# Performance work log

Measured on AMD Instinct MI355X. Metric: run time of the kernel, lower is better.

Reference implementation:

```python
import jax, jax.numpy as jnp
import numpy as np

B, T, D_MODEL = 2, 2048, 2048
N_HEADS, N_KV = 16, 8
HEAD_DIM = D_MODEL // N_HEADS  # 128
EPS = 1e-6


def rmsnorm(x, g):
    # qwen-compatible: compute in fp32, scale by learned weight
    xf = x.astype(jnp.float32)
    var = jnp.mean(xf * xf, axis=-1, keepdims=True)
    return (xf * jax.lax.rsqrt(var + EPS) * g).astype(x.dtype)


def apply_rope(x, cos, sin):
    # x: [b, h, t, d]; cos/sin: [t, d]
    d = x.shape[-1]
    x1, x2 = x[..., : d // 2], x[..., d // 2 :]
    rotated = jnp.concatenate([-x2, x1], axis=-1)
    return x * cos[None, None, :, :] + rotated * sin[None, None, :, :]


def setup_inputs() -> dict:
    key = jax.random.key(0)
    ks = jax.random.split(key, 8)
    x = jax.random.normal(ks[0], (B, T, D_MODEL), dtype=jnp.float32)
    # causal mask: True = masked out
    mask = jnp.triu(jnp.ones((T, T), dtype=bool), k=1)
    # rope tables
    inv_freq = 1.0 / (1e6 ** (np.arange(0, HEAD_DIM, 2, dtype=np.float32) / HEAD_DIM))
    angles = np.arange(T, dtype=np.float32)[:, None] * inv_freq[None, :]  # [T, d/2]
    angles = np.concatenate([angles, angles], axis=1)  # [T, d]
    cos = jnp.asarray(np.cos(angles), dtype=jnp.float32)
    sin = jnp.asarray(np.sin(angles), dtype=jnp.float32)
    s = 0.02
    Wq = jax.random.normal(ks[1], (D_MODEL, D_MODEL), dtype=jnp.float32) * s
    Wk = jax.random.normal(ks[2], (N_KV * HEAD_DIM, D_MODEL), dtype=jnp.float32) * s
    Wv = jax.random.normal(ks[3], (N_KV * HEAD_DIM, D_MODEL), dtype=jnp.float32) * s
    Wo = jax.random.normal(ks[4], (D_MODEL, D_MODEL), dtype=jnp.float32) * s
    bo = jnp.zeros((D_MODEL,), dtype=jnp.float32)
    gq = jnp.ones((HEAD_DIM,), dtype=jnp.float32)
    gk = jnp.ones((HEAD_DIM,), dtype=jnp.float32)
    return {"x": x, "mask": mask, "cos": cos, "sin": sin, "Wq": Wq, "Wk": Wk,
            "Wv": Wv, "Wo": Wo, "bo": bo, "gq": gq, "gk": gk}


def reference(x, mask, cos, sin, Wq, Wk, Wv, Wo, bo, gq, gk):
    b, t, _ = x.shape
    # projections
    q = (x @ Wq.T).reshape(b, t, N_HEADS, HEAD_DIM)
    q = rmsnorm(q, gq).transpose(0, 2, 1, 3)          # [b, H, t, d]
    q = apply_rope(q, cos[:t], sin[:t])
    k = (x @ Wk.T).reshape(b, t, N_KV, HEAD_DIM)
    k = rmsnorm(k, gk).transpose(0, 2, 1, 3)          # [b, G, t, d]
    k = apply_rope(k, cos[:t], sin[:t])
    v = (x @ Wv.T).reshape(b, t, N_KV, HEAD_DIM).transpose(0, 2, 1, 3)
    # GQA broadcast of KV heads
    rep = N_HEADS // N_KV
    k = jnp.repeat(k, rep, axis=1)                    # [b, H, t, d]
    v = jnp.repeat(v, rep, axis=1)
    scores = jnp.einsum("bhqd,bhkd->bhqk", q, k)
    scores = jnp.where(mask[:t, :t][None, None], -jnp.inf, scores)
    attn = jax.nn.softmax(scores / jnp.sqrt(jnp.float32(HEAD_DIM)), axis=-1)
    out = jnp.einsum("bhqk,bhkd->bqhd", attn, v).reshape(b, t, N_HEADS * HEAD_DIM)
    return out @ Wo.T + bo
```

## Files before the change

kernel.cpp:

```cpp
#include <hip/hip_runtime.h>
#include <stdint.h>

#define B_ 2
#define T_ 2048
#define DM 2048
#define NH 16
#define NKV 8
#define HD 128
#define NQKV 4096
#define SC2_ 0.12753102765f

typedef float fx4 __attribute__((ext_vector_type(4)));
typedef float fx16 __attribute__((ext_vector_type(16)));
typedef __bf16 bfx8 __attribute__((ext_vector_type(8)));
typedef unsigned int ux4 __attribute__((ext_vector_type(4)));
typedef unsigned short u16;
typedef unsigned int u32;

typedef __attribute__((address_space(1))) const void gas_t;
typedef __attribute__((address_space(3))) void las_t;

__device__ __forceinline__ u16 f2bf(float f) {
  u32 u = __float_as_uint(f);
  u = (u + 0x7fffu + ((u >> 16) & 1u)) >> 16;
  return (u16)u;
}
__device__ __forceinline__ u32 pk2bf(float lo, float hi) {
  return (u32)f2bf(lo) | ((u32)f2bf(hi) << 16);
}

__device__ __forceinline__ void stage16(const void* g, void* l) {
  __builtin_amdgcn_global_load_lds((gas_t*)(uintptr_t)g, (las_t*)(uintptr_t)l,
                                   16, 0, 0);
}

__global__ void k_cvt(const float* __restrict__ in, u16* __restrict__ out, int n) {
  int i = (blockIdx.x * blockDim.x + threadIdx.x) * 4;
  if (i + 3 < n) {
    float4 v = *(const float4*)(in + i);
    u32 w0 = (u32)f2bf(v.x) | ((u32)f2bf(v.y) << 16);
    u32 w1 = (u32)f2bf(v.z) | ((u32)f2bf(v.w) << 16);
    *(uint2*)(out + i) = make_uint2(w0, w1);
  }
}

__global__ __launch_bounds__(512, 2) void k_gemm256(const u16* __restrict__ A,
                                                    const u16* __restrict__ Bm,
                                                    u16* __restrict__ C,
                                                    int M, int N, int K) {
  __shared__ __align__(16) u16 As[2][2][256 * 32];
  __shared__ __align__(16) u16 Bs[2][2][256 * 32];
  const int nbn = N >> 8;
  const int bm = blockIdx.x / nbn, bn = blockIdx.x % nbn;
  const int tid = threadIdx.x;
  const int w = tid >> 6, lane = tid & 63;
  const int wm = w >> 2, wn = w & 3;
  const int lr = lane & 15, lg = lane >> 4;
  const int cw = (lg ^ ((lr >> 1) & 3)) * 8;
  const u16* Ab = A + (size_t)bm * 256 * K;
  const u16* Bb = Bm + (size_t)bn * 256 * K;
  const int NT = K >> 6;

  auto stage = [&](const u16* gb, u16* region, int tile, int kh) {
#pragma unroll
    for (int i = 0; i < 2; i++) {
      int q = tid + i * 512;
      int row = q >> 2, ch = q & 3;
      int sc = ch ^ ((row >> 1) & 3);
      stage16(gb + (size_t)row * K + tile * 64 + kh * 32 + sc * 8, region + q * 8);
    }
  };

  fx4 acc[8][4];
  const fx4 zero4 = {0.f, 0.f, 0.f, 0.f};
#pragma unroll
  for (int m = 0; m < 8; m++)
#pragma unroll
    for (int n = 0; n < 4; n++) acc[m][n] = zero4;

  stage(Ab, &As[0][0][0], 0, 0);
  stage(Bb, &Bs[0][0][0], 0, 0);
  stage(Ab, &As[0][1][0], 0, 1);
  stage(Bb, &Bs[0][1][0], 0, 1);
  stage(Ab, &As[1][0][0], 1, 0);
  stage(Bb, &Bs[1][0][0], 1, 0);
  asm volatile("s_waitcnt vmcnt(4)" ::: "memory");
  __builtin_amdgcn_s_barrier();

  const int arow = (wm * 128 + lr) * 32;
  const int brow = (wn * 64 + lr) * 32;
  bfx8 af[4], bf[4];

#pragma unroll 1
  for (int t = 0; t < NT; t++) {
    const u16* A0 = &As[t & 1][0][0];
    const u16* A1 = &As[t & 1][1][0];
    const u16* B0 = &Bs[t & 1][0][0];
    const u16* B1 = &Bs[t & 1][1][0];
    const int p1 = (t + 1) & 1, p2 = t & 1;

#pragma unroll
    for (int mi = 0; mi < 4; mi++) af[mi] = *(const bfx8*)(A0 + arow + mi * 512 + cw);
#pragma unroll
    for (int n = 0; n < 4; n++) bf[n] = *(const bfx8*)(B0 + brow + n * 512 + cw);
    if (t + 1 < NT) stage(Ab, &As[p1][1][0], t + 1, 1);
    __builtin_amdgcn_s_barrier();
    asm volatile("s_waitcnt lgkmcnt(0)" ::: "memory");
    __builtin_amdgcn_sched_barrier(0);
    __builtin_amdgcn_s_setprio(1);
#pragma unroll
    for (int mi = 0; mi < 4; mi++)
#pragma unroll
      for (int n = 0; n < 4; n++)
        acc[mi][n] = __builtin_amdgcn_mfma_f32_16x16x32_bf16(af[mi], bf[n], acc[mi][n], 0, 0, 0);
    __builtin_amdgcn_s_setprio(0);
    __builtin_amdgcn_s_barrier();

#pragma unroll
    for (int mi = 0; mi < 4; mi++)
      af[mi] = *(const bfx8*)(A0 + arow + 2048 + mi * 512 + cw);
    if (t + 1 < NT) stage(Bb, &Bs[p1][1][0], t + 1, 1);
    __builtin_amdgcn_s_barrier();
    asm volatile("s_waitcnt lgkmcnt(0)" ::: "memory");
    __builtin_amdgcn_sched_barrier(0);
    __builtin_amdgcn_s_setprio(1);
#pragma unroll
    for (int mi = 0; mi < 4; mi++)
#pragma unroll
      for (int n = 0; n < 4; n++)
        acc[4 + mi][n] = __builtin_amdgcn_mfma_f32_16x16x32_bf16(af[mi], bf[n], acc[4 + mi][n], 0, 0, 0);
    __builtin_amdgcn_s_setprio(0);
    __builtin_amdgcn_s_barrier();

#pragma unroll
    for (int mi = 0; mi < 4; mi++) af[mi] = *(const bfx8*)(A1 + arow + mi * 512 + cw);
#pragma unroll
    for (int n = 0; n < 4; n++) bf[n] = *(const bfx8*)(B1 + brow + n * 512 + cw);
    if (t + 2 < NT) stage(Ab, &As[p2][0][0], t + 2, 0);
    __builtin_amdgcn_s_barrier();
    asm volatile("s_waitcnt lgkmcnt(0)" ::: "memory");
    __builtin_amdgcn_sched_barrier(0);
    __builtin_amdgcn_s_setprio(1);
#pragma unroll
    for (int mi = 0; mi < 4; mi++)
#pragma unroll
      for (int n = 0; n < 4; n++)
        acc[mi][n] = __builtin_amdgcn_mfma_f32_16x16x32_bf16(af[mi], bf[n], acc[mi][n], 0, 0, 0);
    __builtin_amdgcn_s_setprio(0);
    __builtin_amdgcn_s_barrier();

#pragma unroll
    for (int mi = 0; mi < 4; mi++)
      af[mi] = *(const bfx8*)(A1 + arow + 2048 + mi * 512 + cw);
    if (t + 2 < NT) stage(Bb, &Bs[p2][0][0], t + 2, 0);
    __builtin_amdgcn_s_barrier();
    asm volatile("s_waitcnt lgkmcnt(0)" ::: "memory");
    __builtin_amdgcn_sched_barrier(0);
    __builtin_amdgcn_s_setprio(1);
#pragma unroll
    for (int mi = 0; mi < 4; mi++)
#pragma unroll
      for (int n = 0; n < 4; n++)
        acc[4 + mi][n] = __builtin_amdgcn_mfma_f32_16x16x32_bf16(af[mi], bf[n], acc[4 + mi][n], 0, 0, 0);
    __builtin_amdgcn_s_setprio(0);
    asm volatile("s_waitcnt vmcnt(4)" ::: "memory");
    __builtin_amdgcn_s_barrier();
  }

  const int r0 = bm * 256 + wm * 128, c0 = bn * 256 + wn * 64;
#pragma unroll
  for (int m = 0; m < 8; m++) {
#pragma unroll
    for (int n = 0; n < 4; n++) {
      int c = c0 + n * 16 + lr;
#pragma unroll
      for (int i = 0; i < 4; i++)
        C[(size_t)(r0 + m * 16 + lg * 4 + i) * N + c] = f2bf(acc[m][n][i]);
    }
  }
}

template <bool OUT_F32>
__global__ __launch_bounds__(256, 2) void k_gemm(const u16* __restrict__ A,
                                                 const u16* __restrict__ Bm,
                                                 void* __restrict__ Cv,
                                                 const float* __restrict__ bias,
                                                 int M, int N, int K) {
  __shared__ __align__(16) u16 As[128 * 32];
  __shared__ __align__(16) u16 Bs[128 * 32];
  const int nbn = N >> 7;
  const int bm = blockIdx.x / nbn, bn = blockIdx.x % nbn;
  const int tid = threadIdx.x;
  const int w = tid >> 6, lane = tid & 63;
  const int wr = w >> 1, wc = w & 1;
  const int lr = lane & 15, lg = lane >> 4;
  const u16* Ab = A + (size_t)bm * 128 * K;
  const u16* Bb = Bm + (size_t)bn * 128 * K;
  const int srow = lane >> 2, skc = (lane & 3) * 8;

  fx4 zero4 = {0.f, 0.f, 0.f, 0.f};
  fx4 acc[4][4];
#pragma unroll
  for (int m = 0; m < 4; m++)
#pragma unroll
    for (int n = 0; n < 4; n++) acc[m][n] = zero4;

  for (int k0 = 0; k0 < K; k0 += 32) {
#pragma unroll
    for (int t = 0; t < 2; t++) {
      int s = w + t * 4;
      stage16(Ab + (size_t)(s * 16 + srow) * K + k0 + skc, As + s * 512 + lane * 8);
      stage16(Bb + (size_t)(s * 16 + srow) * K + k0 + skc, Bs + s * 512 + lane * 8);
    }
    __syncthreads();
    bfx8 af[4], bfr[4];
#pragma unroll
    for (int m = 0; m < 4; m++)
      af[m] = *(const bfx8*)(As + (wr * 64 + m * 16 + lr) * 32 + lg * 8);
#pragma unroll
    for (int n = 0; n < 4; n++)
      bfr[n] = *(const bfx8*)(Bs + (wc * 64 + n * 16 + lr) * 32 + lg * 8);
#pragma unroll
    for (int m = 0; m < 4; m++)
#pragma unroll
      for (int n = 0; n < 4; n++)
        acc[m][n] = __builtin_amdgcn_mfma_f32_16x16x32_bf16(af[m], bfr[n], acc[m][n], 0, 0, 0);
    __syncthreads();
  }

  const int r0 = bm * 128 + wr * 64, c0 = bn * 128 + wc * 64;
#pragma unroll
  for (int m = 0; m < 4; m++) {
#pragma unroll
    for (int n = 0; n < 4; n++) {
      int c = c0 + n * 16 + lr;
#pragma unroll
      for (int i = 0; i < 4; i++) {
        int r = r0 + m * 16 + lg * 4 + i;
        if (OUT_F32) {
          ((float*)Cv)[(size_t)r * N + c] = acc[m][n][i] + bias[c];
        } else {
          ((u16*)Cv)[(size_t)r * N + c] = f2bf(acc[m][n][i]);
        }
      }
    }
  }
}

__global__ __launch_bounds__(256) void k_qkpost(const u16* __restrict__ qkv,
                                                const float* __restrict__ cosp,
                                                const float* __restrict__ sinp,
                                                const float* __restrict__ gq,
                                                const float* __restrict__ gk,
                                                u16* __restrict__ Qo,
                                                u16* __restrict__ Ko) {
  int bi = blockIdx.x;
  int hh = bi % 24;
  int t64 = (bi / 24) % 32;
  int b = bi / 768;
  int tid = threadIdx.x;
  int j = tid >> 2, p = tid & 3;
  int t = t64 * 64 + j;
  bool isq = hh < 16;
  int colbase = isq ? hh * 128 : 2048 + (hh - 16) * 128;
  const u16* src = qkv + ((size_t)(b * T_ + t)) * NQKV + colbase + p * 32;

  float xv[32];
#pragma unroll
  for (int c = 0; c < 4; c++) {
    uint4 raw = *(const uint4*)(src + c * 8);
    u32 wd[4] = {raw.x, raw.y, raw.z, raw.w};
#pragma unroll
    for (int q2 = 0; q2 < 4; q2++) {
      xv[c * 8 + q2 * 2 + 0] = __uint_as_float(wd[q2] << 16);
      xv[c * 8 + q2 * 2 + 1] = __uint_as_float(wd[q2] & 0xffff0000u);
    }
  }
  float ss = 0.f;
#pragma unroll
  for (int i = 0; i < 32; i++) ss += xv[i] * xv[i];
  ss += __shfl_xor(ss, 1);
  ss += __shfl_xor(ss, 2);
  float rinv = rsqrtf(ss * (1.0f / 128.0f) + 1e-6f);
  const float* g = isq ? gq : gk;
  const float* cr = cosp + (size_t)t * 128 + p * 32;
  const float* sr = sinp + (size_t)t * 128 + p * 32;

  float ov[32];
#pragma unroll
  for (int i = 0; i < 32; i++) {
    float y = xv[i] * rinv * g[p * 32 + i];
    float oth = __shfl_xor(y, 2);
    float rot = (p < 2) ? -oth : oth;
    ov[i] = y * cr[i] + rot * sr[i];
  }

  uint4 pk[4];
#pragma unroll
  for (int c = 0; c < 4; c++) {
    u32 wd[4];
#pragma unroll
    for (int q2 = 0; q2 < 4; q2++)
      wd[q2] = (u32)f2bf(ov[c * 8 + q2 * 2]) | ((u32)f2bf(ov[c * 8 + q2 * 2 + 1]) << 16);
    pk[c] = make_uint4(wd[0], wd[1], wd[2], wd[3]);
  }

  if (isq) {
    u16* dst = Qo + (((size_t)(b * NH + hh)) * T_ + t) * HD + p * 32;
#pragma unroll
    for (int c = 0; c < 4; c++) *(uint4*)(dst + c * 8) = pk[c];
  } else {
    int hk = hh - 16;
    u16* dstrow = Ko + (((size_t)(b * NKV + hk)) * T_ + t) * HD;
#pragma unroll
    for (int c = 0; c < 4; c++) {
      int C = p * 4 + c;
      int Cs = C ^ (t & 7);
      *(uint4*)(dstrow + Cs * 8) = pk[c];
    }
  }
}

__global__ __launch_bounds__(256) void k_vtr(const u16* __restrict__ qkv,
                                             u16* __restrict__ vt) {
  __shared__ __align__(16) u16 sm[128 * 64];
  int bi = blockIdx.x;
  int hv = bi & 7;
  int t64 = (bi >> 3) & 31;
  int b = bi >> 8;
  int tid = threadIdx.x;
#pragma unroll
  for (int it = 0; it < 4; it++) {
    int idx = tid + it * 256;
    int tok = idx >> 4, c = idx & 15;
    uint4 raw = *(const uint4*)(qkv + ((size_t)(b * T_ + t64 * 64 + tok)) * NQKV +
                                3072 + hv * 128 + c * 8);
    u32 wd[4] = {raw.x, raw.y, raw.z, raw.w};
#pragma unroll
    for (int q2 = 0; q2 < 4; q2++) {
      sm[(c * 8 + q2 * 2 + 0) * 64 + tok] = (u16)(wd[q2] & 0xffffu);
      sm[(c * 8 + q2 * 2 + 1) * 64 + tok] = (u16)(wd[q2] >> 16);
    }
  }
  __syncthreads();
  int d = tid >> 1, half = tid & 1;
  size_t rowb = (((size_t)(b * NKV + hv)) * HD + d) * T_ + t64 * 64;
#pragma unroll
  for (int c = 0; c < 4; c++) {
    int cg = half * 4 + c;
    int cs = cg ^ (d & 7);
    u32 wd[4];
#pragma unroll
    for (int q2 = 0; q2 < 4; q2++) {
      u32 lo = sm[d * 64 + half * 32 + c * 8 + 2 * q2];
      u32 hi = sm[d * 64 + half * 32 + c * 8 + 2 * q2 + 1];
      wd[q2] = lo | (hi << 16);
    }
    *(uint4*)(vt + rowb + cs * 8) = make_uint4(wd[0], wd[1], wd[2], wd[3]);
  }
}

__global__ __launch_bounds__(256, 2) void k_attn(const u16* __restrict__ Qg,
                                                 const u16* __restrict__ Kg,
                                                 const u16* __restrict__ Vg,
                                                 u16* __restrict__ Og) {
  __shared__ __align__(16) u16 Ks[2][64 * 128];
  __shared__ __align__(16) u16 Vs[2][128 * 64];
  const int bi = blockIdx.x;
  const int zr = bi & 15, h = (bi >> 4) & 15, b = bi >> 8;
  const int z = b ? (15 - zr) : zr;
  const int hkv = h >> 1;
  const int tid = threadIdx.x, w = tid >> 6, lane = tid & 63;
  const int q31 = lane & 31, H8 = lane >> 5;
  const int sel = ((w >> 1) ^ bi) & 1;
  const int zt = sel ? (31 - z) : z;
  const int qr0 = zt * 64 + (w & 1) * 32;
  const int qg = qr0 + q31;
  const int nch = 32 - z;
  const int myl = zt + 1;

  const u16* kb = Kg + ((size_t)(b * NKV + hkv)) * T_ * HD;
  const u16* vb = Vg + ((size_t)(b * NKV + hkv)) * HD * T_;

  const u16* qrow = Qg + (((size_t)(b * NH + h)) * T_ + qg) * HD;
  bfx8 qf[8];
#pragma unroll
  for (int step = 0; step < 8; step++)
    qf[step] = *(const bfx8*)(qrow + step * 16 + H8 * 8);

  fx16 o[4];
  const fx16 zero16 = {0.f, 0.f, 0.f, 0.f, 0.f, 0.f, 0.f, 0.f,
                       0.f, 0.f, 0.f, 0.f, 0.f, 0.f, 0.f, 0.f};
#pragma unroll
  for (int db = 0; db < 4; db++) o[db] = zero16;
  float l_i = 0.f;

  auto stageKV = [&](int buf, int kv0) {
    u16* Kd = &Ks[buf][0];
    u16* Vd = &Vs[buf][0];
#pragma unroll
    for (int it = 0; it < 4; it++) {
      int r = it * 16 + (tid >> 4);
      stage16(kb + (size_t)(kv0 + r) * HD + (tid & 15) * 8, Kd + it * 2048 + tid * 8);
      int d = it * 32 + (tid >> 3);
      stage16(vb + (size_t)d * T_ + kv0 + (tid & 7) * 8, Vd + it * 2048 + tid * 8);
    }
  };

  stageKV(0, 0);
  asm volatile("s_waitcnt vmcnt(0)" ::: "memory");
  __builtin_amdgcn_s_barrier();
  int cur = 0;

#pragma unroll 1
  for (int ch = 0; ch < nch; ch++) {
    if (ch + 1 < nch) {
      stageKV(cur ^ 1, (ch + 1) * 64);
      asm volatile("s_waitcnt vmcnt(8)" ::: "memory");
    } else {
      asm volatile("s_waitcnt vmcnt(0)" ::: "memory");
    }
    __builtin_amdgcn_s_barrier();

    if (ch < myl) {
      const u16* Kd = &Ks[cur][0];
      const u16* Vd = &Vs[cur][0];
      const int kv0 = ch * 64;
      const bool diag = (ch == zt);

#pragma unroll
      for (int kvb = 0; kvb < 2; kvb++) {
        const int krow = kvb * 32 + q31;
        const u16* kr = Kd + krow * 128;
        fx16 st = zero16;
        __builtin_amdgcn_s_setprio(1);
#pragma unroll
        for (int step = 0; step < 8; step++) {
          int cs = ((step << 1) | H8) ^ (krow & 7);
          bfx8 kf = *(const bfx8*)(kr + cs * 8);
          st = __builtin_amdgcn_mfma_f32_32x32x16_bf16(kf, qf[step], st, 0, 0, 0);
        }
        __builtin_amdgcn_s_setprio(0);

        float pv[16];
#pragma unroll
        for (int r = 0; r < 16; r++) {
          float p = exp2f(st[r] * SC2_);
          if (diag) {
            int kvg = kv0 + kvb * 32 + (r & 3) + 8 * (r >> 2) + 4 * H8;
            p = (kvg > qg) ? 0.f : p;
          }
          l_i += p;
          pv[r] = p;
        }

#pragma unroll
        for (int half = 0; half < 2; half++) {
          const int rb = half * 8;
          u32 A0 = pk2bf(pv[rb + 0], pv[rb + 1]);
          u32 A1 = pk2bf(pv[rb + 2], pv[rb + 3]);
          u32 B0 = pk2bf(pv[rb + 4], pv[rb + 5]);
          u32 B1 = pk2bf(pv[rb + 6], pv[rb + 7]);
          asm volatile("v_permlane32_swap_b32 %0, %1" : "+v"(A0), "+v"(B0));
          asm volatile("v_permlane32_swap_b32 %0, %1" : "+v"(A1), "+v"(B1));
          union { ux4 u; bfx8 b; } pa;
          pa.u = (ux4){A0, A1, B0, B1};
          const int ks = kvb * 2 + half;
          __builtin_amdgcn_s_setprio(1);
#pragma unroll
          for (int db = 0; db < 4; db++) {
            int vrow = db * 32 + q31;
            int cv = ((ks << 1) | H8) ^ (vrow & 7);
            bfx8 vf = *(const bfx8*)(Vd + vrow * 64 + cv * 8);
            o[db] = __builtin_amdgcn_mfma_f32_32x32x16_bf16(vf, pa.b, o[db], 0, 0, 0);
          }
          __builtin_amdgcn_s_setprio(0);
        }
      }
    }
    __builtin_amdgcn_s_barrier();
    cur ^= 1;
  }

  float lt = l_i + __shfl_xor(l_i, 32);
  float inv = 1.0f / lt;
  u16* ob = Og + ((size_t)(b * T_ + qg)) * DM + h * HD;
#pragma unroll
  for (int db = 0; db < 4; db++) {
#pragma unroll
    for (int g = 0; g < 4; g++) {
      int d0 = db * 32 + 8 * g + 4 * H8;
      u32 w0 = pk2bf(o[db][4 * g + 0] * inv, o[db][4 * g + 1] * inv);
      u32 w1 = pk2bf(o[db][4 * g + 2] * inv, o[db][4 * g + 3] * inv);
      *(uint2*)(ob + d0) = make_uint2(w0, w1);
    }
  }
}

extern "C" void kernel_launch(void* const* d_in, const int* in_sizes, int n_in,
                              void* d_out, int out_size, void* d_ws, size_t ws_size,
                              hipStream_t stream) {
  const float* x = (const float*)d_in[0];
  const float* cosp = (const float*)d_in[2];
  const float* sinp = (const float*)d_in[3];
  const float* Wq = (const float*)d_in[4];
  const float* Wk = (const float*)d_in[5];
  const float* Wv = (const float*)d_in[6];
  const float* Wo = (const float*)d_in[7];
  const float* bo = (const float*)d_in[8];
  const float* gq = (const float*)d_in[9];
  const float* gk = (const float*)d_in[10];

  char* ws = (char*)d_ws;
  u16* xbf  = (u16*)(ws + 0);
  u16* wqkv = (u16*)(ws + 16777216);
  u16* wo   = (u16*)(ws + 33554432);
  u16* qkv  = (u16*)(ws + 41943040);
  u16* qb   = (u16*)(ws + 75497472);
  u16* kb   = (u16*)(ws + 92274688);
  u16* vt   = (u16*)(ws + 100663296);
  u16* ab   = (u16*)(ws + 109051904);
  float* out = (float*)d_out;

  k_cvt<<<8192, 256, 0, stream>>>(x, xbf, 8388608);
  k_cvt<<<4096, 256, 0, stream>>>(Wq, wqkv, 4194304);
  k_cvt<<<2048, 256, 0, stream>>>(Wk, wqkv + 4194304, 2097152);
  k_cvt<<<2048, 256, 0, stream>>>(Wv, wqkv + 6291456, 2097152);
  k_cvt<<<4096, 256, 0, stream>>>(Wo, wo, 4194304);

  k_gemm256<<<256, 512, 0, stream>>>(xbf, wqkv, qkv, 4096, 4096, 2048);
  k_qkpost<<<1536, 256, 0, stream>>>(qkv, cosp, sinp, gq, gk, qb, kb);
  k_vtr<<<512, 256, 0, stream>>>(qkv, vt);
  k_attn<<<512, 256, 0, stream>>>(qb, kb, vt, ab);
  k_gemm<true><<<512, 256, 0, stream>>>(ab, wo, out, bo, 4096, 2048, 2048);
}
```

Measured before the change: 267.2 us.

## Split KV tile across wave pairs in attention and reduce partials via LDS

Doubles the attention block to 512 threads so each pair of waves shares the same query rows but processes different 32-row halves of each 64-row KV chunk. Partial output accumulators and row sums from one half are written to the reused K/V shared buffers and added by the other half before normalization and store. This shortens each wave's serial MFMA chain and raises the number of waves in flight. In exchange it adds an LDS reduction pass, a block-wide sync, and more register pressure under the tighter launch bounds.

```diff
diff --git a/kernel.cpp b/kernel.cpp
--- a/kernel.cpp
+++ b/kernel.cpp
@@ -360,24 +360,26 @@
   }
 }
 
-__global__ __launch_bounds__(256, 2) void k_attn(const u16* __restrict__ Qg,
+__global__ __launch_bounds__(512, 2) void k_attn(const u16* __restrict__ Qg,
                                                  const u16* __restrict__ Kg,
                                                  const u16* __restrict__ Vg,
                                                  u16* __restrict__ Og) {
   __shared__ __align__(16) u16 Ks[2][64 * 128];
   __shared__ __align__(16) u16 Vs[2][128 * 64];
+  __shared__ float lb[4][32];
   const int bi = blockIdx.x;
   const int zr = bi & 15, h = (bi >> 4) & 15, b = bi >> 8;
   const int z = b ? (15 - zr) : zr;
   const int hkv = h >> 1;
   const int tid = threadIdx.x, w = tid >> 6, lane = tid & 63;
   const int q31 = lane & 31, H8 = lane >> 5;
-  const int sel = ((w >> 1) ^ bi) & 1;
-  const int zt = sel ? (31 - z) : z;
-  const int qr0 = zt * 64 + (w & 1) * 32;
+  const int kvh = w & 1, rh = (w >> 1) & 1, thi = w >> 2;
+  const int zt = thi ? (31 - z) : z;
+  const int qr0 = zt * 64 + rh * 32;
   const int qg = qr0 + q31;
   const int nch = 32 - z;
   const int myl = zt + 1;
+  const int pair = w >> 1;
 
   const u16* kb = Kg + ((size_t)(b * NKV + hkv)) * T_ * HD;
   const u16* vb = Vg + ((size_t)(b * NKV + hkv)) * HD * T_;
@@ -399,11 +401,11 @@
     u16* Kd = &Ks[buf][0];
     u16* Vd = &Vs[buf][0];
 #pragma unroll
-    for (int it = 0; it < 4; it++) {
-      int r = it * 16 + (tid >> 4);
-      stage16(kb + (size_t)(kv0 + r) * HD + (tid & 15) * 8, Kd + it * 2048 + tid * 8);
-      int d = it * 32 + (tid >> 3);
-      stage16(vb + (size_t)d * T_ + kv0 + (tid & 7) * 8, Vd + it * 2048 + tid * 8);
+    for (int it = 0; it < 2; it++) {
+      int r = it * 32 + (tid >> 4);
+      stage16(kb + (size_t)(kv0 + r) * HD + (tid & 15) * 8, Kd + it * 4096 + tid * 8);
+      int d = it * 64 + (tid >> 3);
+      stage16(vb + (size_t)d * T_ + kv0 + (tid & 7) * 8, Vd + it * 4096 + tid * 8);
     }
   };
 
@@ -416,7 +418,7 @@
   for (int ch = 0; ch < nch; ch++) {
     if (ch + 1 < nch) {
       stageKV(cur ^ 1, (ch + 1) * 64);
-      asm volatile("s_waitcnt vmcnt(8)" ::: "memory");
+      asm volatile("s_waitcnt vmcnt(4)" ::: "memory");
     } else {
       asm volatile("s_waitcnt vmcnt(0)" ::: "memory");
     }
@@ -428,54 +430,51 @@
       const int kv0 = ch * 64;
       const bool diag = (ch == zt);
 
-#pragma unroll
-      for (int kvb = 0; kvb < 2; kvb++) {
-        const int krow = kvb * 32 + q31;
-        const u16* kr = Kd + krow * 128;
-        fx16 st = zero16;
+      const int krow = kvh * 32 + q31;
+      const u16* kr = Kd + krow * 128;
+      fx16 st = zero16;
+      __builtin_amdgcn_s_setprio(1);
+#pragma unroll
+      for (int step = 0; step < 8; step++) {
+        int cs = ((step << 1) | H8) ^ (krow & 7);
+        bfx8 kf = *(const bfx8*)(kr + cs * 8);
+        st = __builtin_amdgcn_mfma_f32_32x32x16_bf16(kf, qf[step], st, 0, 0, 0);
+      }
+      __builtin_amdgcn_s_setprio(0);
+
+      float pv[16];
+#pragma unroll
+      for (int r = 0; r < 16; r++) {
+        float p = exp2f(st[r] * SC2_);
+        if (diag) {
+          int kvg = kv0 + kvh * 32 + (r & 3) + 8 * (r >> 2) + 4 * H8;
+          p = (kvg > qg) ? 0.f : p;
+        }
+        l_i += p;
+        pv[r] = p;
+      }
+
+#pragma unroll
+      for (int half = 0; half < 2; half++) {
+        const int rb = half * 8;
+        u32 A0 = pk2bf(pv[rb + 0], pv[rb + 1]);
+        u32 A1 = pk2bf(pv[rb + 2], pv[rb + 3]);
+        u32 B0 = pk2bf(pv[rb + 4], pv[rb + 5]);
+        u32 B1 = pk2bf(pv[rb + 6], pv[rb + 7]);
+        asm volatile("v_permlane32_swap_b32 %0, %1" : "+v"(A0), "+v"(B0));
+        asm volatile("v_permlane32_swap_b32 %0, %1" : "+v"(A1), "+v"(B1));
+        union { ux4 u; bfx8 b; } pa;
+        pa.u = (ux4){A0, A1, B0, B1};
+        const int ks = kvh * 2 + half;
         __builtin_amdgcn_s_setprio(1);
 #pragma unroll
-        for (int step = 0; step < 8; step++) {
-          int cs = ((step << 1) | H8) ^ (krow & 7);
-          bfx8 kf = *(const bfx8*)(kr + cs * 8);
-          st = __builtin_amdgcn_mfma_f32_32x32x16_bf16(kf, qf[step], st, 0, 0, 0);
+        for (int db = 0; db < 4; db++) {
+          int vrow = db * 32 + q31;
+          int cv = ((ks << 1) | H8) ^ (vrow & 7);
+          bfx8 vf = *(const bfx8*)(Vd + vrow * 64 + cv * 8);
+          o[db] = __builtin_amdgcn_mfma_f32_32x32x16_bf16(vf, pa.b, o[db], 0, 0, 0);
         }
         __builtin_amdgcn_s_setprio(0);
-
-        float pv[16];
-#pragma unroll
-        for (int r = 0; r < 16; r++) {
-          float p = exp2f(st[r] * SC2_);
-          if (diag) {
-            int kvg = kv0 + kvb * 32 + (r & 3) + 8 * (r >> 2) + 4 * H8;
-            p = (kvg > qg) ? 0.f : p;
-          }
-          l_i += p;
-          pv[r] = p;
-        }
-
-#pragma unroll
-        for (int half = 0; half < 2; half++) {
-          const int rb = half * 8;
-          u32 A0 = pk2bf(pv[rb + 0], pv[rb + 1]);
-          u32 A1 = pk2bf(pv[rb + 2], pv[rb + 3]);
-          u32 B0 = pk2bf(pv[rb + 4], pv[rb + 5]);
-          u32 B1 = pk2bf(pv[rb + 6], pv[rb + 7]);
-          asm volatile("v_permlane32_swap_b32 %0, %1" : "+v"(A0), "+v"(B0));
-          asm volatile("v_permlane32_swap_b32 %0, %1" : "+v"(A1), "+v"(B1));
-          union { ux4 u; bfx8 b; } pa;
-          pa.u = (ux4){A0, A1, B0, B1};
-          const int ks = kvb * 2 + half;
-          __builtin_amdgcn_s_setprio(1);
-#pragma unroll
-          for (int db = 0; db < 4; db++) {
-            int vrow = db * 32 + q31;
-            int cv = ((ks << 1) | H8) ^ (vrow & 7);
-            bfx8 vf = *(const bfx8*)(Vd + vrow * 64 + cv * 8);
-            o[db] = __builtin_amdgcn_mfma_f32_32x32x16_bf16(vf, pa.b, o[db], 0, 0, 0);
-          }
-          __builtin_amdgcn_s_setprio(0);
-        }
       }
     }
     __builtin_amdgcn_s_barrier();
@@ -483,16 +482,34 @@
   }
 
   float lt = l_i + __shfl_xor(l_i, 32);
-  float inv = 1.0f / lt;
-  u16* ob = Og + ((size_t)(b * T_ + qg)) * DM + h * HD;
-#pragma unroll
-  for (int db = 0; db < 4; db++) {
-#pragma unroll
-    for (int g = 0; g < 4; g++) {
-      int d0 = db * 32 + 8 * g + 4 * H8;
-      u32 w0 = pk2bf(o[db][4 * g + 0] * inv, o[db][4 * g + 1] * inv);
-      u32 w1 = pk2bf(o[db][4 * g + 2] * inv, o[db][4 * g + 3] * inv);
-      *(uint2*)(ob + d0) = make_uint2(w0, w1);
+  float* cb = (pair < 2) ? ((float*)&Ks[0][0] + pair * 4096)
+                         : ((float*)&Vs[0][0] + (pair - 2) * 4096);
+  if (kvh == 1) {
+    if (H8 == 0) lb[pair][q31] = lt;
+#pragma unroll
+    for (int db = 0; db < 4; db++)
+#pragma unroll
+      for (int g = 0; g < 4; g++) {
+        int dofs = (db * 32 + 8 * g + 4 * H8) ^ ((q31 & 7) << 2);
+        *(fx4*)(cb + q31 * 128 + dofs) =
+            (fx4){o[db][4 * g], o[db][4 * g + 1], o[db][4 * g + 2], o[db][4 * g + 3]};
+      }
+  }
+  __syncthreads();
+  if (kvh == 0) {
+    float inv = 1.0f / (lt + lb[pair][q31]);
+    u16* ob = Og + ((size_t)(b * T_ + qg)) * DM + h * HD;
+#pragma unroll
+    for (int db = 0; db < 4; db++) {
+#pragma unroll
+      for (int g = 0; g < 4; g++) {
+        int dofs = (db * 32 + 8 * g + 4 * H8) ^ ((q31 & 7) << 2);
+        fx4 op = *(const fx4*)(cb + q31 * 128 + dofs);
+        int d0 = db * 32 + 8 * g + 4 * H8;
+        u32 w0 = pk2bf((o[db][4 * g] + op[0]) * inv, (o[db][4 * g + 1] + op[1]) * inv);
+        u32 w1 = pk2bf((o[db][4 * g + 2] + op[2]) * inv, (o[db][4 * g + 3] + op[3]) * inv);
+        *(uint2*)(ob + d0) = make_uint2(w0, w1);
+      }
     }
   }
 }
@@ -531,6 +548,6 @@
   k_gemm256<<<256, 512, 0, stream>>>(xbf, wqkv, qkv, 4096, 4096, 2048);
   k_qkpost<<<1536, 256, 0, stream>>>(qkv, cosp, sinp, gq, gk, qb, kb);
   k_vtr<<<512, 256, 0, stream>>>(qkv, vt);
-  k_attn<<<512, 256, 0, stream>>>(qb, kb, vt, ab);
+  k_attn<<<512, 512, 0, stream>>>(qb, kb, vt, ab);
   k_gemm<true><<<512, 256, 0, stream>>>(ab, wo, out, bo, 4096, 2048, 2048);
 }
```

New measurement: 266.5 us. Within noise of the previous version (-0.3%).
